# Performance work log

Measured on AMD Instinct MI355X. Metric: run time of the kernel, lower is better.

## Reference

```python
import jax, jax.numpy as jnp
import numpy as np

NX = 1024
N_HEAD = 16
HEAD_DIM = NX // N_HEAD
MASKED_BIAS = -10000.0


def setup_inputs() -> dict:
    key = jax.random.key(0)
    k1, k2, k3 = jax.random.split(key, 3)
    hidden_states = jax.random.normal(k1, (2, 2048, NX), dtype=jnp.float32)
    # Conv1D weights: stored [in, out], y = x @ W + b (like torch addmm)
    c_attn_w = jax.random.normal(k2, (NX, 3 * NX), dtype=jnp.float32) * 0.02
    c_attn_b = jnp.zeros((3 * NX,), dtype=jnp.float32)
    c_proj_w = jax.random.normal(k3, (NX, NX), dtype=jnp.float32) * 0.02
    c_proj_b = jnp.zeros((NX,), dtype=jnp.float32)
    return {
        "hidden_states": hidden_states,
        "c_attn_w": c_attn_w,
        "c_attn_b": c_attn_b,
        "c_proj_w": c_proj_w,
        "c_proj_b": c_proj_b,
    }


def reference(hidden_states, c_attn_w, c_attn_b, c_proj_w, c_proj_b):
    B, S, _ = hidden_states.shape
    qkv = hidden_states @ c_attn_w + c_attn_b  # [B, S, 3*NX]
    q, k, v = jnp.split(qkv, 3, axis=-1)
    # split heads -> [B, H, S, D]
    def split_heads(x):
        return x.reshape(B, S, N_HEAD, HEAD_DIM).transpose(0, 2, 1, 3)
    q, k, v = split_heads(q), split_heads(k), split_heads(v)
    # scores scaled by sqrt(head_dim) (v.size(-1)**0.5 in original)
    w = jnp.einsum("bhqd,bhkd->bhqk", q, k) / jnp.sqrt(jnp.float32(HEAD_DIM))
    # causal mask (nd == ns here since no past)
    causal = jnp.tril(jnp.ones((S, S), dtype=bool))
    w = jnp.where(causal[None, None, :, :], w, jnp.float32(MASKED_BIAS))
    w = jax.nn.softmax(w, axis=-1)
    a = jnp.einsum("bhqk,bhkd->bhqd", w, v)  # [B, H, S, D]
    # merge heads
    a = a.transpose(0, 2, 1, 3).reshape(B, S, NX)
    out = a @ c_proj_w + c_proj_b
    return out
```

## Files before the change

### kernel.cpp

```cpp
#include <hip/hip_runtime.h>
#include <hip/hip_bf16.h>
#include <cmath>

typedef __attribute__((ext_vector_type(8))) short bf16x8;
typedef __attribute__((ext_vector_type(4))) float f32x4;

#define NXC 1024
#define NH 16
#define HD 64
#define BATCH 2
#define SEQ 2048
#define TOK (BATCH * SEQ)

__device__ __forceinline__ ushort f2bf(float f) {
  unsigned u;
  asm("v_cvt_pk_bf16_f32 %0, %1, %2" : "=v"(u) : "v"(f), "v"(f));
  return (ushort)u;
}

__device__ __forceinline__ void gload_lds16(const void* g, void* lds) {
  __builtin_amdgcn_global_load_lds(
      (const __attribute__((address_space(1))) void*)g,
      (__attribute__((address_space(3))) void*)lds, 16, 0, 0);
}

__device__ __forceinline__ float fast_exp2(float x) {
  float r;
  asm("v_exp_f32 %0, %1" : "=v"(r) : "v"(x));
  return r;
}

template <int CTRL>
__device__ __forceinline__ float dpp_mov(float x) {
  return __builtin_bit_cast(
      float, __builtin_amdgcn_mov_dpp(__builtin_bit_cast(int, x), CTRL, 0xF, 0xF, true));
}
__device__ __forceinline__ float red16_max(float x) {
  x = fmaxf(x, dpp_mov<0x121>(x));
  x = fmaxf(x, dpp_mov<0x122>(x));
  x = fmaxf(x, dpp_mov<0x124>(x));
  x = fmaxf(x, dpp_mov<0x128>(x));
  return x;
}
__device__ __forceinline__ float red16_sum(float x) {
  x += dpp_mov<0x121>(x);
  x += dpp_mov<0x122>(x);
  x += dpp_mov<0x124>(x);
  x += dpp_mov<0x128>(x);
  return x;
}

__global__ __launch_bounds__(256) void k_transpose_w(const float* __restrict__ in,
                                                     ushort* __restrict__ out,
                                                     int Kd, int Nd) {
  __shared__ float t[32][33];
  int n0 = blockIdx.x * 32, k0 = blockIdx.y * 32;
  int tx = threadIdx.x & 31, ty = threadIdx.x >> 5;
#pragma unroll
  for (int r = 0; r < 4; ++r)
    t[tx][ty + r * 8] = in[(size_t)(k0 + ty + r * 8) * Nd + n0 + tx];
  __syncthreads();
  int nl = threadIdx.x >> 3, kq = (threadIdx.x & 7) * 4;
  ushort4 o;
  o.x = f2bf(t[nl][kq + 0]);
  o.y = f2bf(t[nl][kq + 1]);
  o.z = f2bf(t[nl][kq + 2]);
  o.w = f2bf(t[nl][kq + 3]);
  int row = n0 + nl, kk = k0 + kq;
  size_t dst = (size_t)row * Kd + (kk & ~63) + ((kk & 63) ^ ((row & 7) << 3));
  *(ushort4*)&out[dst] = o;
}

__global__ __launch_bounds__(256) void k_transpose_v(const ushort* __restrict__ in,
                                                     ushort* __restrict__ out) {
  __shared__ ushort t[32][33];
  int bh = blockIdx.z;
  int s0 = blockIdx.x * 32, d0 = blockIdx.y * 32;
  const ushort* ip = in + (size_t)bh * SEQ * HD;
  ushort* op = out + (size_t)bh * HD * SEQ;
  int tx = threadIdx.x & 31, ty = threadIdx.x >> 5;
#pragma unroll
  for (int r = 0; r < 4; ++r)
    t[tx][ty + r * 8] = ip[(size_t)(s0 + ty + r * 8) * HD + d0 + tx];
  __syncthreads();
  int dl = threadIdx.x >> 3, sq = (threadIdx.x & 7) * 4;
  ushort4 o;
  o.x = t[dl][sq + 0]; o.y = t[dl][sq + 1];
  o.z = t[dl][sq + 2]; o.w = t[dl][sq + 3];
  int key = (s0 + sq) ^ ((dl & 7) << 3);
  *(ushort4*)&op[(size_t)(d0 + dl) * SEQ + key] = o;
}

__global__ __launch_bounds__(256, 3) void k_gemm_qkv(const float* __restrict__ X,
                                                     const ushort* __restrict__ Bt,
                                                     const float* __restrict__ bias,
                                                     ushort* __restrict__ q_ws,
                                                     ushort* __restrict__ k_ws,
                                                     ushort* __restrict__ v_tmp) {
  __shared__ ushort As[128 * 64];
  __shared__ ushort Bs[2][128 * 64];
  const int tid = threadIdx.x;
  const int wave = tid >> 6, lane = tid & 63;
  const int xcd = blockIdx.x & 7, loc = blockIdx.x >> 3;
  const int m0 = ((xcd >> 1) * 8 + (loc & 7)) * 128;
  const int n0 = ((xcd & 1) * 12 + (loc >> 3)) * 128;
  const int wr = (wave >> 1) * 64, wc = (wave & 1) * 64;
  const int l15 = lane & 15, lg = lane >> 4;
  const int swz = (l15 & 7) << 3;
  const int arow = wave * 32 + lg;
  const int akcol = l15 * 4;
  f32x4 acc[4][4] = {};
  float4 areg[8];

  auto a_issue = [&](int kt) {
#pragma unroll
    for (int c = 0; c < 8; ++c)
      areg[c] = *(const float4*)&X[(size_t)(m0 + arow + c * 4) * 1024 + kt * 64 + akcol];
  };
  auto a_write = [&]() {
#pragma unroll
    for (int c = 0; c < 8; ++c) {
      int row = arow + c * 4;
      unsigned p0, p1;
      asm("v_cvt_pk_bf16_f32 %0, %1, %2" : "=v"(p0) : "v"(areg[c].x), "v"(areg[c].y));
      asm("v_cvt_pk_bf16_f32 %0, %1, %2" : "=v"(p1) : "v"(areg[c].z), "v"(areg[c].w));
      *(uint2*)&As[row * 64 + (akcol ^ ((row & 7) << 3))] = make_uint2(p0, p1);
    }
  };
  auto stageB = [&](int kt, int buf) {
#pragma unroll
    for (int c = 0; c < 4; ++c) {
      int offB = wave * 4096 + c * 1024 + lane * 16;
      int row = offB >> 7, colB = offB & 127;
      gload_lds16((const char*)Bt + (size_t)(n0 + row) * 2048 + kt * 128 + colB,
                  (char*)Bs[buf] + wave * 4096 + c * 1024);
    }
  };

  a_issue(0);
  stageB(0, 0);
  a_write();
  a_issue(1);
  asm volatile("s_waitcnt vmcnt(8) lgkmcnt(0)" ::: "memory");
  __builtin_amdgcn_s_barrier();

#pragma unroll 1
  for (int kt = 0; kt < 16; ++kt) {
    const int cur = kt & 1;
    if (kt < 15) stageB(kt + 1, cur ^ 1);
#pragma unroll
    for (int kc = 0; kc < 2; ++kc) {
      bf16x8 af[4], bfr[4];
#pragma unroll
      for (int i = 0; i < 4; ++i)
        af[i] = *(const bf16x8*)&As[(wr + i * 16 + l15) * 64 + ((kc * 32 + lg * 8) ^ swz)];
#pragma unroll
      for (int j = 0; j < 4; ++j)
        bfr[j] = *(const bf16x8*)&Bs[cur][(wc + j * 16 + l15) * 64 + ((kc * 32 + lg * 8) ^ swz)];
#pragma unroll
      for (int i = 0; i < 4; ++i)
#pragma unroll
        for (int j = 0; j < 4; ++j)
          acc[i][j] = __builtin_amdgcn_mfma_f32_16x16x32_bf16(af[i], bfr[j], acc[i][j], 0, 0, 0);
    }
    __syncthreads();
    if (kt < 15) {
      a_write();
      if (kt < 14) a_issue(kt + 2);
      asm volatile("s_waitcnt lgkmcnt(0)" ::: "memory");
      __builtin_amdgcn_s_barrier();
    }
  }

#pragma unroll
  for (int j = 0; j < 4; ++j) {
    int col = n0 + wc + j * 16 + l15;
    float bv = bias[col];
    int sec = col >> 10;
    int within = col & 1023;
    int head = within >> 6, d = within & 63;
#pragma unroll
    for (int i = 0; i < 4; ++i) {
#pragma unroll
      for (int r = 0; r < 4; ++r) {
        int row = m0 + wr + i * 16 + lg * 4 + r;
        int b = row >> 11, s = row & 2047;
        float val = acc[i][j][r] + bv;
        size_t hb = ((size_t)(b * NH + head) * SEQ + s) * HD;
        if (sec == 0)      q_ws[hb + d] = f2bf(val * 0.1803368801f);
        else if (sec == 1) k_ws[hb + (d ^ ((s & 7) << 3))] = f2bf(val);
        else               v_tmp[hb + d] = f2bf(val);
      }
    }
  }
}

__global__ __launch_bounds__(256) void k_attn(const ushort* __restrict__ q_ws,
                                              const ushort* __restrict__ k_ws,
                                              const ushort* __restrict__ v_ws,
                                              ushort* __restrict__ a_ws) {
  __shared__ ushort Ks[2][64 * 64];
  __shared__ ushort Vs[2][64 * 64];
  __shared__ ushort Ps[4][2][16 * 64];
  const int p = blockIdx.x, bh = blockIdx.y;
  const int qtA = 31 - p, qtB = p;
  const int tid = threadIdx.x, wave = tid >> 6, lane = tid & 63;
  const int l15 = lane & 15, lg = lane >> 4;
  const int swz = (l15 & 7) << 3;
  const ushort* qp = q_ws + (size_t)bh * SEQ * HD;
  const ushort* kp = k_ws + (size_t)bh * SEQ * HD;
  const ushort* vp = v_ws + (size_t)bh * HD * SEQ;

  bf16x8 qfA[2], qfB[2];
  {
    int qrA = qtA * 64 + wave * 16 + l15;
    int qrB = qtB * 64 + wave * 16 + l15;
    qfA[0] = *(const bf16x8*)&qp[(size_t)qrA * HD + lg * 8];
    qfA[1] = *(const bf16x8*)&qp[(size_t)qrA * HD + 32 + lg * 8];
    qfB[0] = *(const bf16x8*)&qp[(size_t)qrB * HD + lg * 8];
    qfB[1] = *(const bf16x8*)&qp[(size_t)qrB * HD + 32 + lg * 8];
  }
  f32x4 oA[4] = {}, oB[4] = {};
  float mA[4] = {-INFINITY, -INFINITY, -INFINITY, -INFINITY};
  float mB[4] = {-INFINITY, -INFINITY, -INFINITY, -INFINITY};
  float lA[4] = {0.f, 0.f, 0.f, 0.f}, lB[4] = {0.f, 0.f, 0.f, 0.f};

  auto stage = [&](int kt, int buf) {
#pragma unroll
    for (int c = 0; c < 2; ++c) {
      int offB = wave * 2048 + c * 1024 + lane * 16;
      gload_lds16((const char*)kp + (size_t)kt * 8192 + offB,
                  (char*)Ks[buf] + offB);
      int d = offB >> 7, keyB = offB & 127;
      gload_lds16((const char*)vp + (size_t)d * (SEQ * 2) + (size_t)kt * 128 + keyB,
                  (char*)Vs[buf] + offB);
    }
  };

  auto tile_step = [&](const bf16x8* qf, f32x4* o, float* m_r, float* l_r,
                       ushort* Pw, const ushort* Kc, const ushort* Vc, bool diag) {
    f32x4 sc[4] = {};
#pragma unroll
    for (int kc = 0; kc < 2; ++kc)
#pragma unroll
      for (int f = 0; f < 4; ++f) {
        if (diag && f > wave) continue;
        bf16x8 kf = *(const bf16x8*)&Kc[(f * 16 + l15) * 64 + ((kc * 32 + lg * 8) ^ swz)];
        sc[f] = __builtin_amdgcn_mfma_f32_16x16x32_bf16(qf[kc], kf, sc[f], 0, 0, 0);
      }
    if (diag) {
#pragma unroll
      for (int f = 0; f < 4; ++f) {
        int key_rel = f * 16 + l15;
#pragma unroll
        for (int r = 0; r < 4; ++r) {
          int q_rel = wave * 16 + lg * 4 + r;
          if (key_rel > q_rel) sc[f][r] = -1e30f;
        }
      }
    }
    float pm[4];
#pragma unroll
    for (int r = 0; r < 4; ++r)
      pm[r] = fmaxf(fmaxf(sc[0][r], sc[1][r]), fmaxf(sc[2][r], sc[3][r]));
    bool need = false;
#pragma unroll
    for (int r = 0; r < 4; ++r) need |= (pm[r] > m_r[r] + 8.f);
    if (__any(need)) {
#pragma unroll
      for (int r = 0; r < 4; ++r) {
        float full = red16_max(pm[r]);
        float mn = fmaxf(m_r[r], full);
        float al = fast_exp2(m_r[r] - mn);
        m_r[r] = mn;
        l_r[r] *= al;
#pragma unroll
        for (int df = 0; df < 4; ++df) o[df][r] *= al;
      }
    }
#pragma unroll
    for (int f = 0; f < 4; ++f)
#pragma unroll
      for (int r = 0; r < 4; ++r) {
        float pv = fast_exp2(sc[f][r] - m_r[r]);
        l_r[r] += pv;
        int q = lg * 4 + r;
        Pw[q * 64 + ((f * 16 + l15) ^ ((q & 7) << 3))] = f2bf(pv);
      }
#pragma unroll
    for (int kc = 0; kc < 2; ++kc) {
      bf16x8 pf = *(const bf16x8*)&Pw[l15 * 64 + ((kc * 32 + lg * 8) ^ swz)];
#pragma unroll
      for (int df = 0; df < 4; ++df) {
        bf16x8 vf = *(const bf16x8*)&Vc[(df * 16 + l15) * 64 + ((kc * 32 + lg * 8) ^ swz)];
        o[df] = __builtin_amdgcn_mfma_f32_16x16x32_bf16(pf, vf, o[df], 0, 0, 0);
      }
    }
  };

  stage(0, 0);
  asm volatile("s_waitcnt vmcnt(0)" ::: "memory");
  __syncthreads();

  for (int kt = 0; kt <= qtA; ++kt) {
    const int cur = kt & 1;
    if (kt < qtA) stage(kt + 1, cur ^ 1);
    tile_step(qfA, oA, mA, lA, Ps[wave][0], Ks[cur], Vs[cur], kt == qtA);
    if (kt <= qtB)
      tile_step(qfB, oB, mB, lB, Ps[wave][1], Ks[cur], Vs[cur], kt == qtB);
    asm volatile("s_waitcnt vmcnt(0)" ::: "memory");
    __syncthreads();
  }

  int b = bh >> 4, head = bh & 15;
  auto epilogue = [&](f32x4* o, float* l_r, int qt) {
#pragma unroll
    for (int r = 0; r < 4; ++r) {
      float inv = 1.0f / red16_sum(l_r[r]);
      int s = qt * 64 + wave * 16 + lg * 4 + r;
#pragma unroll
      for (int df = 0; df < 4; ++df) {
        int col = head * 64 + ((df * 16 + l15) ^ ((s & 7) << 3));
        a_ws[((size_t)(b * SEQ + s)) * NXC + col] = f2bf(o[df][r] * inv);
      }
    }
  };
  epilogue(oA, lA, qtA);
  epilogue(oB, lB, qtB);
}

__global__ __launch_bounds__(256) void k_gemm_proj(const ushort* __restrict__ A,
                                                   const ushort* __restrict__ Bt,
                                                   const float* __restrict__ bias,
                                                   float* __restrict__ out) {
  __shared__ ushort As[2][128 * 64];
  __shared__ ushort Bs[2][128 * 64];
  const int tid = threadIdx.x;
  const int wave = tid >> 6, lane = tid & 63;
  const int xcd = blockIdx.x & 7, loc = blockIdx.x >> 3;
  const int m0 = ((xcd >> 1) * 8 + (loc & 7)) * 128;
  const int n0 = ((xcd & 1) * 4 + (loc >> 3)) * 128;
  const int wr = (wave >> 1) * 64, wc = (wave & 1) * 64;
  const int l15 = lane & 15, lg = lane >> 4;
  const int swz = (l15 & 7) << 3;
  f32x4 acc[4][4] = {};

  auto stage = [&](int k0, int buf) {
#pragma unroll
    for (int c = 0; c < 4; ++c) {
      int offB = wave * 4096 + c * 1024 + lane * 16;
      int row = offB >> 7, colB = offB & 127;
      gload_lds16((const char*)A + (size_t)(m0 + row) * 2048 + k0 * 2 + colB,
                  (char*)As[buf] + wave * 4096 + c * 1024);
      gload_lds16((const char*)Bt + (size_t)(n0 + row) * 2048 + k0 * 2 + colB,
                  (char*)Bs[buf] + wave * 4096 + c * 1024);
    }
  };

  stage(0, 0);
  asm volatile("s_waitcnt vmcnt(0)" ::: "memory");
  __syncthreads();

  for (int kt = 0; kt < 16; ++kt) {
    const int cur = kt & 1;
    if (kt < 15) stage((kt + 1) * 64, cur ^ 1);
#pragma unroll
    for (int kc = 0; kc < 2; ++kc) {
      bf16x8 af[4], bfr[4];
#pragma unroll
      for (int i = 0; i < 4; ++i)
        af[i] = *(const bf16x8*)&As[cur][(wr + i * 16 + l15) * 64 + ((kc * 32 + lg * 8) ^ swz)];
#pragma unroll
      for (int j = 0; j < 4; ++j)
        bfr[j] = *(const bf16x8*)&Bs[cur][(wc + j * 16 + l15) * 64 + ((kc * 32 + lg * 8) ^ swz)];
#pragma unroll
      for (int i = 0; i < 4; ++i)
#pragma unroll
        for (int j = 0; j < 4; ++j)
          acc[i][j] = __builtin_amdgcn_mfma_f32_16x16x32_bf16(af[i], bfr[j], acc[i][j], 0, 0, 0);
    }
    asm volatile("s_waitcnt vmcnt(0)" ::: "memory");
    __syncthreads();
  }
#pragma unroll
  for (int j = 0; j < 4; ++j) {
    int col = n0 + wc + j * 16 + l15;
    float bv = bias[col];
#pragma unroll
    for (int i = 0; i < 4; ++i) {
#pragma unroll
      for (int r = 0; r < 4; ++r) {
        int row = m0 + wr + i * 16 + lg * 4 + r;
        out[(size_t)row * NXC + col] = acc[i][j][r] + bv;
      }
    }
  }
}

extern "C" void kernel_launch(void* const* d_in, const int* in_sizes, int n_in,
                              void* d_out, int out_size, void* d_ws, size_t ws_size,
                              hipStream_t stream) {
  const float* hs       = (const float*)d_in[0];
  const float* c_attn_w = (const float*)d_in[1];
  const float* c_attn_b = (const float*)d_in[2];
  const float* c_proj_w = (const float*)d_in[3];
  const float* c_proj_b = (const float*)d_in[4];
  char* ws = (char*)d_ws;
  const size_t MB = 1 << 20;
  ushort* Wt_attn = (ushort*)(ws + 8 * MB);
  ushort* Wt_proj = (ushort*)(ws + 14 * MB);
  ushort* q_ws    = (ushort*)(ws + 16 * MB);
  ushort* k_ws    = (ushort*)(ws + 24 * MB);
  ushort* v_ws    = (ushort*)(ws + 32 * MB);
  ushort* a_ws    = (ushort*)(ws + 40 * MB);
  ushort* v_tmp   = a_ws;

  k_transpose_w<<<dim3(96, 32), 256, 0, stream>>>(c_attn_w, Wt_attn, 1024, 3072);
  k_transpose_w<<<dim3(32, 32), 256, 0, stream>>>(c_proj_w, Wt_proj, 1024, 1024);
  k_gemm_qkv<<<768, 256, 0, stream>>>(hs, Wt_attn, c_attn_b, q_ws, k_ws, v_tmp);
  k_transpose_v<<<dim3(64, 2, 32), 256, 0, stream>>>(v_tmp, v_ws);
  k_attn<<<dim3(16, 32), 256, 0, stream>>>(q_ws, k_ws, v_ws, a_ws);
  k_gemm_proj<<<256, 256, 0, stream>>>(a_ws, Wt_proj, c_proj_b, (float*)d_out);
}
```

Measured before the change: 128.7 us.

## Fuse V transpose into QKV GEMM epilogue and restructure attention inner loop

The QKV GEMM epilogue now writes V directly in the transposed, permuted/swizzled layout the attention kernel expects, so the separate V transpose kernel and its round trip through memory are gone. A key permutation keeps the P store contiguous, letting each lane pack four probabilities into one 8-byte LDS write with paired bf16 conversion. K and V fragments are loaded into registers once per tile and shared by both query tiles. s_setprio is raised around the MFMA blocks, and __syncthreads is replaced by a bare s_barrier. Risks are scattered 2-byte global stores for V in the GEMM epilogue and higher register pressure in the attention kernel.

Measured after the change: 130.9 us. No clear change (+1.7%).

```diff
diff --git a/kernel.cpp b/kernel.cpp
--- a/kernel.cpp
+++ b/kernel.cpp
@@ -71,32 +71,12 @@
   *(ushort4*)&out[dst] = o;
 }
 
-__global__ __launch_bounds__(256) void k_transpose_v(const ushort* __restrict__ in,
-                                                     ushort* __restrict__ out) {
-  __shared__ ushort t[32][33];
-  int bh = blockIdx.z;
-  int s0 = blockIdx.x * 32, d0 = blockIdx.y * 32;
-  const ushort* ip = in + (size_t)bh * SEQ * HD;
-  ushort* op = out + (size_t)bh * HD * SEQ;
-  int tx = threadIdx.x & 31, ty = threadIdx.x >> 5;
-#pragma unroll
-  for (int r = 0; r < 4; ++r)
-    t[tx][ty + r * 8] = ip[(size_t)(s0 + ty + r * 8) * HD + d0 + tx];
-  __syncthreads();
-  int dl = threadIdx.x >> 3, sq = (threadIdx.x & 7) * 4;
-  ushort4 o;
-  o.x = t[dl][sq + 0]; o.y = t[dl][sq + 1];
-  o.z = t[dl][sq + 2]; o.w = t[dl][sq + 3];
-  int key = (s0 + sq) ^ ((dl & 7) << 3);
-  *(ushort4*)&op[(size_t)(d0 + dl) * SEQ + key] = o;
-}
-
 __global__ __launch_bounds__(256, 3) void k_gemm_qkv(const float* __restrict__ X,
                                                      const ushort* __restrict__ Bt,
                                                      const float* __restrict__ bias,
                                                      ushort* __restrict__ q_ws,
                                                      ushort* __restrict__ k_ws,
-                                                     ushort* __restrict__ v_tmp) {
+                                                     ushort* __restrict__ v_ws) {
   __shared__ ushort As[128 * 64];
   __shared__ ushort Bs[2][128 * 64];
   const int tid = threadIdx.x;
@@ -186,10 +166,15 @@
         int row = m0 + wr + i * 16 + lg * 4 + r;
         int b = row >> 11, s = row & 2047;
         float val = acc[i][j][r] + bv;
-        size_t hb = ((size_t)(b * NH + head) * SEQ + s) * HD;
-        if (sec == 0)      q_ws[hb + d] = f2bf(val * 0.1803368801f);
-        else if (sec == 1) k_ws[hb + (d ^ ((s & 7) << 3))] = f2bf(val);
-        else               v_tmp[hb + d] = f2bf(val);
+        int bh = b * NH + head;
+        if (sec == 0) {
+          q_ws[((size_t)bh * SEQ + s) * HD + d] = f2bf(val * 0.1803368801f);
+        } else if (sec == 1) {
+          k_ws[((size_t)bh * SEQ + s) * HD + (d ^ ((s & 7) << 3))] = f2bf(val);
+        } else {
+          int slot = (((s & 15) * 4 + ((s >> 4) & 3)) ^ ((d & 7) << 3));
+          v_ws[((size_t)bh * HD + d) * SEQ + (s & ~63) + slot] = f2bf(val);
+        }
       }
     }
   }
@@ -224,6 +209,7 @@
   float mA[4] = {-INFINITY, -INFINITY, -INFINITY, -INFINITY};
   float mB[4] = {-INFINITY, -INFINITY, -INFINITY, -INFINITY};
   float lA[4] = {0.f, 0.f, 0.f, 0.f}, lB[4] = {0.f, 0.f, 0.f, 0.f};
+  bf16x8 kf[2][4], vf[2][4];
 
   auto stage = [&](int kt, int buf) {
 #pragma unroll
@@ -238,16 +224,17 @@
   };
 
   auto tile_step = [&](const bf16x8* qf, f32x4* o, float* m_r, float* l_r,
-                       ushort* Pw, const ushort* Kc, const ushort* Vc, bool diag) {
+                       ushort* Pw, bool diag) {
     f32x4 sc[4] = {};
+    __builtin_amdgcn_s_setprio(1);
 #pragma unroll
     for (int kc = 0; kc < 2; ++kc)
 #pragma unroll
       for (int f = 0; f < 4; ++f) {
         if (diag && f > wave) continue;
-        bf16x8 kf = *(const bf16x8*)&Kc[(f * 16 + l15) * 64 + ((kc * 32 + lg * 8) ^ swz)];
-        sc[f] = __builtin_amdgcn_mfma_f32_16x16x32_bf16(qf[kc], kf, sc[f], 0, 0, 0);
-      }
+        sc[f] = __builtin_amdgcn_mfma_f32_16x16x32_bf16(qf[kc], kf[kc][f], sc[f], 0, 0, 0);
+      }
+    __builtin_amdgcn_s_setprio(0);
     if (diag) {
 #pragma unroll
       for (int f = 0; f < 4; ++f) {
@@ -279,23 +266,27 @@
       }
     }
 #pragma unroll
-    for (int f = 0; f < 4; ++f)
-#pragma unroll
-      for (int r = 0; r < 4; ++r) {
-        float pv = fast_exp2(sc[f][r] - m_r[r]);
-        l_r[r] += pv;
-        int q = lg * 4 + r;
-        Pw[q * 64 + ((f * 16 + l15) ^ ((q & 7) << 3))] = f2bf(pv);
-      }
+    for (int r = 0; r < 4; ++r) {
+      int q = lg * 4 + r;
+      float e0 = fast_exp2(sc[0][r] - m_r[r]);
+      float e1 = fast_exp2(sc[1][r] - m_r[r]);
+      float e2 = fast_exp2(sc[2][r] - m_r[r]);
+      float e3 = fast_exp2(sc[3][r] - m_r[r]);
+      l_r[r] += (e0 + e1) + (e2 + e3);
+      unsigned p0, p1;
+      asm("v_cvt_pk_bf16_f32 %0, %1, %2" : "=v"(p0) : "v"(e0), "v"(e1));
+      asm("v_cvt_pk_bf16_f32 %0, %1, %2" : "=v"(p1) : "v"(e2), "v"(e3));
+      *(uint2*)&Pw[q * 64 + ((l15 * 4) ^ ((q & 7) << 3))] = make_uint2(p0, p1);
+    }
+    __builtin_amdgcn_s_setprio(1);
 #pragma unroll
     for (int kc = 0; kc < 2; ++kc) {
       bf16x8 pf = *(const bf16x8*)&Pw[l15 * 64 + ((kc * 32 + lg * 8) ^ swz)];
 #pragma unroll
-      for (int df = 0; df < 4; ++df) {
-        bf16x8 vf = *(const bf16x8*)&Vc[(df * 16 + l15) * 64 + ((kc * 32 + lg * 8) ^ swz)];
-        o[df] = __builtin_amdgcn_mfma_f32_16x16x32_bf16(pf, vf, o[df], 0, 0, 0);
-      }
-    }
+      for (int df = 0; df < 4; ++df)
+        o[df] = __builtin_amdgcn_mfma_f32_16x16x32_bf16(pf, vf[kc][df], o[df], 0, 0, 0);
+    }
+    __builtin_amdgcn_s_setprio(0);
   };
 
   stage(0, 0);
@@ -305,11 +296,18 @@
   for (int kt = 0; kt <= qtA; ++kt) {
     const int cur = kt & 1;
     if (kt < qtA) stage(kt + 1, cur ^ 1);
-    tile_step(qfA, oA, mA, lA, Ps[wave][0], Ks[cur], Vs[cur], kt == qtA);
+#pragma unroll
+    for (int kc = 0; kc < 2; ++kc)
+#pragma unroll
+      for (int f = 0; f < 4; ++f) {
+        kf[kc][f] = *(const bf16x8*)&Ks[cur][(f * 16 + l15) * 64 + ((kc * 32 + lg * 8) ^ swz)];
+        vf[kc][f] = *(const bf16x8*)&Vs[cur][(f * 16 + l15) * 64 + ((kc * 32 + lg * 8) ^ swz)];
+      }
+    tile_step(qfA, oA, mA, lA, Ps[wave][0], kt == qtA);
     if (kt <= qtB)
-      tile_step(qfB, oB, mB, lB, Ps[wave][1], Ks[cur], Vs[cur], kt == qtB);
+      tile_step(qfB, oB, mB, lB, Ps[wave][1], kt == qtB);
     asm volatile("s_waitcnt vmcnt(0)" ::: "memory");
-    __syncthreads();
+    __builtin_amdgcn_s_barrier();
   }
 
   int b = bh >> 4, head = bh & 15;
@@ -413,12 +411,10 @@
   ushort* k_ws    = (ushort*)(ws + 24 * MB);
   ushort* v_ws    = (ushort*)(ws + 32 * MB);
   ushort* a_ws    = (ushort*)(ws + 40 * MB);
-  ushort* v_tmp   = a_ws;
 
   k_transpose_w<<<dim3(96, 32), 256, 0, stream>>>(c_attn_w, Wt_attn, 1024, 3072);
   k_transpose_w<<<dim3(32, 32), 256, 0, stream>>>(c_proj_w, Wt_proj, 1024, 1024);
-  k_gemm_qkv<<<768, 256, 0, stream>>>(hs, Wt_attn, c_attn_b, q_ws, k_ws, v_tmp);
-  k_transpose_v<<<dim3(64, 2, 32), 256, 0, stream>>>(v_tmp, v_ws);
+  k_gemm_qkv<<<768, 256, 0, stream>>>(hs, Wt_attn, c_attn_b, q_ws, k_ws, v_ws);
   k_attn<<<dim3(16, 32), 256, 0, stream>>>(q_ws, k_ws, v_ws, a_ws);
   k_gemm_proj<<<256, 256, 0, stream>>>(a_ws, Wt_proj, c_proj_b, (float*)d_out);
 }
```
